# Performance work log

Hardware: AMD Instinct MI355X
Metric: run time of the kernel (lower is better)

## Reference

```python
import jax, jax.numpy as jnp
import numpy as np

EMBED = 1024
HEADS = 16
HEAD_DIM = EMBED // HEADS


def setup_inputs() -> dict:
    key = jax.random.key(0)
    k1, k2, k3, k4, k5 = jax.random.split(key, 5)
    B, S = 4, 2048
    scale = 1.0 / np.sqrt(EMBED)
    return {
        "query_features": jax.random.normal(k1, (B, S, EMBED), dtype=jnp.float32),
        "W_qkv": jax.random.normal(k2, (EMBED, 3 * EMBED), dtype=jnp.float32) * scale,
        "b_qkv": jnp.zeros((3 * EMBED,), dtype=jnp.float32),
        "W_out": jax.random.normal(k3, (EMBED, EMBED), dtype=jnp.float32) * scale,
        "b_out": jnp.zeros((EMBED,), dtype=jnp.float32),
    }


def reference(query_features, W_qkv, b_qkv, W_out, b_out):
    B, S, E = query_features.shape
    qkv = jnp.einsum("bse,ef->bsf", query_features, W_qkv) + b_qkv  # [B,S,3E]
    q, k, v = jnp.split(qkv, 3, axis=-1)
    # split heads: [B,H,S,D]
    def heads(x):
        return x.reshape(B, S, HEADS, HEAD_DIM).transpose(0, 2, 1, 3)
    q, k, v = heads(q), heads(k), heads(v)
    scale = 1.0 / np.sqrt(HEAD_DIM)
    scores = jnp.einsum("bhqd,bhkd->bhqk", q, k) * scale
    attn = jax.nn.softmax(scores, axis=-1)
    out = jnp.einsum("bhqk,bhkd->bhqd", attn, v)  # [B,H,S,D]
    out = out.transpose(0, 2, 1, 3).reshape(B, S, E)
    return jnp.einsum("bse,ef->bsf", out, W_out) + b_out
```

## Files before the change

### kernel.cpp

```cpp
#include <hip/hip_runtime.h>
#include <hip/hip_bf16.h>
#include <stdint.h>
#include <stddef.h>

using short8  = __attribute__((ext_vector_type(8))) short;
using short4v = __attribute__((ext_vector_type(4))) short;
using int4v   = __attribute__((ext_vector_type(4))) int;
using f32x4   = __attribute__((ext_vector_type(4))) float;
typedef __hip_bfloat16 bf16_t;

__device__ __forceinline__ void glds16(const void* g, const void* l) {
  __builtin_amdgcn_global_load_lds(
      (const __attribute__((address_space(1))) void*)g,
      (__attribute__((address_space(3))) void*)l, 16, 0, 0);
}
__device__ __forceinline__ short bfbits(float x) {
  bf16_t h = __float2bfloat16(x);
  return __builtin_bit_cast(short, h);
}
__device__ __forceinline__ int pk2(float lo, float hi) {
  return __builtin_amdgcn_perm(__builtin_bit_cast(unsigned, hi),
                               __builtin_bit_cast(unsigned, lo), 0x07060302u);
}

__global__ __launch_bounds__(256)
void preprocess(const void* __restrict__ Wqkv, bf16_t* __restrict__ WqkvT,
                const void* __restrict__ Wout, bf16_t* __restrict__ WoutT,
                const void* __restrict__ Xv, bf16_t* __restrict__ Xb,
                int* __restrict__ flag) {
  __shared__ int sbad;
  __shared__ float tile[32][33];
  const int tid = threadIdx.x;
  const int bid = blockIdx.x;
  if (tid == 0) sbad = 0;
  __syncthreads();
  {
    int bad = 0;
    const unsigned short* wp = (const unsigned short*)Wqkv;
#pragma unroll
    for (int j = 0; j < 4; ++j) {
      float f = __uint_as_float((unsigned)wp[tid + j * 256] << 16);
      if (!(fabsf(f) <= 1e10f)) bad = 1;
    }
    if (bad) sbad = 1;
  }
  __syncthreads();
  const int isf = sbad;
  if (bid == 0 && tid == 0) *flag = isf;

  if (bid < 4096) {
    int bx = bid & 127;
    const int by = bid >> 7;
    const int tx = tid & 31, ty = tid >> 5;
    const void* Wv;
    bf16_t* Wt;
    int C;
    if (bx < 96) {
      Wv = Wqkv; Wt = WqkvT; C = 3072;
    } else {
      bx -= 96; Wv = Wout; Wt = WoutT; C = 1024;
    }
    const int n0 = bx * 32, k0 = by * 32;
#pragma unroll
    for (int j = 0; j < 4; ++j) {
      const int k = k0 + ty + j * 8;
      tile[ty + j * 8][tx] =
          isf ? ((const float*)Wv)[(size_t)k * C + n0 + tx]
              : __bfloat162float(((const bf16_t*)Wv)[(size_t)k * C + n0 + tx]);
    }
    __syncthreads();
#pragma unroll
    for (int j = 0; j < 4; ++j) {
      const int n = n0 + ty + j * 8;
      Wt[(size_t)n * 1024 + k0 + tx] = __float2bfloat16(tile[tx][ty + j * 8]);
    }
  } else {
    const int i = ((bid - 4096) * 256 + tid) * 4;
    if (isf) {
      const float4 v = *(const float4*)((const float*)Xv + i);
      Xb[i + 0] = __float2bfloat16(v.x);
      Xb[i + 1] = __float2bfloat16(v.y);
      Xb[i + 2] = __float2bfloat16(v.z);
      Xb[i + 3] = __float2bfloat16(v.w);
    } else {
      *(uint2*)(Xb + i) = *(const uint2*)((const bf16_t*)Xv + i);
    }
  }
}

template <int MODE>
__global__ __launch_bounds__(256)
void gemm_k(const bf16_t* __restrict__ A, const bf16_t* __restrict__ Bt,
            const void* __restrict__ biasv, void* __restrict__ Cv,
            bf16_t* __restrict__ Qo, bf16_t* __restrict__ Ko,
            bf16_t* __restrict__ Vo, int M, int N, int K,
            const int* __restrict__ flag) {
  constexpr float CSC = 0.18033688011112042f;
  __shared__ __align__(16) bf16_t lA[2][128 * 64];
  __shared__ __align__(16) bf16_t lB[2][128 * 64];

  const int isf32 = *flag;
  const int tid  = threadIdx.x;
  const int w    = tid >> 6;
  const int lane = tid & 63;
  const int lrow = lane & 15;
  const int quad = lane >> 4;
  const int m0 = blockIdx.x * 128;
  const int n0 = blockIdx.y * 128;
  const int wm = (w >> 1) * 64;
  const int wn = (w & 1) * 64;

  f32x4 acc[4][4];
  for (int i = 0; i < 4; ++i)
    for (int j = 0; j < 4; ++j)
      for (int r = 0; r < 4; ++r) acc[i][j][r] = 0.f;

  const char* Ab = (const char*)A;
  const char* Bb = (const char*)Bt;
  unsigned aoff[4], boff[4];
  int ldst[4];
#pragma unroll
  for (int i = 0; i < 4; ++i) {
    const int cbase = i * 256 + w * 64;
    const int c = cbase + lane;
    const int row = c >> 3;
    const int q = (c & 7) ^ (row & 7);
    aoff[i] = (unsigned)((m0 + row) * K + q * 8) * 2u;
    boff[i] = (unsigned)((n0 + row) * K + q * 8) * 2u;
    ldst[i] = cbase * 16;
  }

  auto stage = [&](int buf, int kt) {
    const unsigned kb = (unsigned)kt * 2u;
#pragma unroll
    for (int i = 0; i < 4; ++i) {
      glds16(Ab + aoff[i] + kb, (const char*)lA[buf] + ldst[i]);
      glds16(Bb + boff[i] + kb, (const char*)lB[buf] + ldst[i]);
    }
  };

  stage(0, 0);
  __syncthreads();

  int buf = 0;
  for (int kt = 0; kt < K; kt += 64) {
    if (kt + 64 < K) stage(buf ^ 1, kt + 64);
    const char* la = (const char*)lA[buf];
    const char* lb = (const char*)lB[buf];
#pragma unroll
    for (int ks = 0; ks < 2; ++ks) {
      short8 af[4], bfr[4];
#pragma unroll
      for (int mi = 0; mi < 4; ++mi) {
        const int row = wm + mi * 16 + lrow;
        const int slot = (ks * 4 + quad) ^ (row & 7);
        af[mi] = *(const short8*)(la + row * 128 + slot * 16);
      }
#pragma unroll
      for (int ni = 0; ni < 4; ++ni) {
        const int row = wn + ni * 16 + lrow;
        const int slot = (ks * 4 + quad) ^ (row & 7);
        bfr[ni] = *(const short8*)(lb + row * 128 + slot * 16);
      }
#pragma unroll
      for (int mi = 0; mi < 4; ++mi)
#pragma unroll
        for (int ni = 0; ni < 4; ++ni)
          acc[mi][ni] = __builtin_amdgcn_mfma_f32_16x16x32_bf16(
              af[mi], bfr[ni], acc[mi][ni], 0, 0, 0);
    }
    __syncthreads();
    buf ^= 1;
  }

  if (MODE == 1) {
    const int sec = n0 >> 10;
    const int b = m0 >> 11;
    const int s0 = (m0 & 2047) + wm + quad * 4;
#pragma unroll
    for (int mi = 0; mi < 4; ++mi) {
#pragma unroll
      for (int ni = 0; ni < 4; ++ni) {
        const int col = n0 + wn + ni * 16 + lrow;
        const float bv = isf32 ? ((const float*)biasv)[col]
                               : __bfloat162float(((const bf16_t*)biasv)[col]);
        const int h = (col >> 6) & 15, d = col & 63;
        const int s = s0 + mi * 16;
        if (sec == 2) {
          short4v hv4;
#pragma unroll
          for (int r = 0; r < 4; ++r) hv4[r] = bfbits(acc[mi][ni][r] + bv);
          *(short4v*)(Vo + ((((size_t)b * 16 + h) * 64) + d) * 2048 + s) = hv4;
        } else if (sec == 0) {
          bf16_t* dst = Qo + ((((size_t)b * 16 + h) * 2048) + s) * 64 + d;
#pragma unroll
          for (int r = 0; r < 4; ++r)
            dst[(size_t)r * 64] = __float2bfloat16((acc[mi][ni][r] + bv) * CSC);
        } else {
          bf16_t* dst = Ko + ((((size_t)b * 16 + h) * 2048) + s) * 64 + d;
#pragma unroll
          for (int r = 0; r < 4; ++r)
            dst[(size_t)r * 64] = __float2bfloat16(acc[mi][ni][r] + bv);
        }
      }
    }
  } else {
#pragma unroll
    for (int mi = 0; mi < 4; ++mi) {
#pragma unroll
      for (int ni = 0; ni < 4; ++ni) {
        const int col = n0 + wn + ni * 16 + lrow;
        const float bv = isf32 ? ((const float*)biasv)[col]
                               : __bfloat162float(((const bf16_t*)biasv)[col]);
#pragma unroll
        for (int r = 0; r < 4; ++r) {
          const int row = m0 + wm + mi * 16 + quad * 4 + r;
          const float val = acc[mi][ni][r] + bv;
          if (isf32)
            ((float*)Cv)[(size_t)row * N + col] = val;
          else
            ((bf16_t*)Cv)[(size_t)row * N + col] = __float2bfloat16(val);
        }
      }
    }
  }
}

__global__ __launch_bounds__(256, 2)
void attn_fwd(const bf16_t* __restrict__ Q, const bf16_t* __restrict__ K,
              const bf16_t* __restrict__ Vt, bf16_t* __restrict__ AO) {
  __shared__ __align__(16) bf16_t lK[2][64 * 64];
  __shared__ __align__(16) bf16_t lV[2][64 * 64];

  const int tid  = threadIdx.x;
  const int w    = tid >> 6;
  const int lane = tid & 63;
  const int lrow = lane & 15;
  const int quad = lane >> 4;
  const int id = blockIdx.x;
  const int swz = (id & 7) * 64 + (id >> 3);
  const int bh  = swz >> 3;
  const int q0  = (swz & 7) * 256;

  const bf16_t* Qb = Q + (size_t)bh * 2048 * 64;
  const char* Kbc = (const char*)(K + (size_t)bh * 2048 * 64);
  const char* Vbc = (const char*)(Vt + (size_t)bh * 64 * 2048);

  const int rbase = (lrow >> 2) * 8 + (lrow & 3);
  const int fkl   = 2 * (lrow >> 2) + (lrow & 1);

  short8 aq[4][2];
#pragma unroll
  for (int qt = 0; qt < 4; ++qt)
#pragma unroll
    for (int ks = 0; ks < 2; ++ks)
      aq[qt][ks] = *(const short8*)(Qb +
          (size_t)(q0 + w * 64 + qt * 16 + lrow) * 64 + ks * 32 + quad * 8);

  short8 ones;
#pragma unroll
  for (int j = 0; j < 8; ++j) ones[j] = (short)0x3F80;

  const f32x4 zf = {0.f, 0.f, 0.f, 0.f};

  f32x4 ot[4][4];
  f32x4 lsacc[4];
#pragma unroll
  for (int dt = 0; dt < 4; ++dt)
#pragma unroll
    for (int qt = 0; qt < 4; ++qt)
#pragma unroll
      for (int r = 0; r < 4; ++r) ot[dt][qt][r] = 0.f;
#pragma unroll
  for (int qt = 0; qt < 4; ++qt)
#pragma unroll
    for (int r = 0; r < 4; ++r) lsacc[qt][r] = 0.f;

  unsigned kgo[2], vgo[2];
  int ldst[2];
#pragma unroll
  for (int i = 0; i < 2; ++i) {
    const int cbase = i * 256 + w * 64;
    const int c = cbase + lane;
    const int row = c >> 3, ch = c & 7;
    const int fk = 2 * ((row >> 3) & 3) + (row & 1);
    kgo[i] = (unsigned)(row * 128 + (ch ^ fk) * 16);
    vgo[i] = (unsigned)(row * 4096 + (ch ^ (row & 7)) * 16);
    ldst[i] = cbase * 16;
  }

  auto stage = [&](int buf, int cidx) {
    const unsigned kb = (unsigned)cidx * 8192u;
    const unsigned vb = (unsigned)cidx * 128u;
#pragma unroll
    for (int i = 0; i < 2; ++i) {
      glds16(Kbc + kgo[i] + kb, (const char*)lK[buf] + ldst[i]);
      glds16(Vbc + vgo[i] + vb, (const char*)lV[buf] + ldst[i]);
    }
  };

  auto compute = [&](const bf16_t* lKb, const bf16_t* lVb) {
#pragma unroll
    for (int g = 0; g < 2; ++g) {
      short8 ak0[2], ak1[2];
#pragma unroll
      for (int T = 0; T < 2; ++T) {
        const int row = g * 32 + T * 4 + rbase;
        ak0[T] = *(const short8*)((const char*)lKb + row * 128 +
                                  ((0 * 4 + quad) ^ fkl) * 16);
        ak1[T] = *(const short8*)((const char*)lKb + row * 128 +
                                  ((1 * 4 + quad) ^ fkl) * 16);
      }
      f32x4 sc[2][4];
      __builtin_amdgcn_s_setprio(1);
#pragma unroll
      for (int T = 0; T < 2; ++T)
#pragma unroll
        for (int qt = 0; qt < 4; ++qt)
          sc[T][qt] = __builtin_amdgcn_mfma_f32_16x16x32_bf16(
              ak0[T], aq[qt][0], zf, 0, 0, 0);
#pragma unroll
      for (int T = 0; T < 2; ++T)
#pragma unroll
        for (int qt = 0; qt < 4; ++qt)
          sc[T][qt] = __builtin_amdgcn_mfma_f32_16x16x32_bf16(
              ak1[T], aq[qt][1], sc[T][qt], 0, 0, 0);
      __builtin_amdgcn_s_setprio(0);

      short8 pb[4];
#pragma unroll
      for (int qt = 0; qt < 4; ++qt) {
        float p[8];
#pragma unroll
        for (int T = 0; T < 2; ++T)
#pragma unroll
          for (int r = 0; r < 4; ++r)
            p[T * 4 + r] = __builtin_amdgcn_exp2f(sc[T][qt][r]);
        int4v pi = {pk2(p[0], p[1]), pk2(p[2], p[3]), pk2(p[4], p[5]),
                    pk2(p[6], p[7])};
        pb[qt] = __builtin_bit_cast(short8, pi);
      }

      __builtin_amdgcn_s_setprio(1);
#pragma unroll
      for (int qt = 0; qt < 4; ++qt)
        lsacc[qt] = __builtin_amdgcn_mfma_f32_16x16x32_bf16(ones, pb[qt],
                                                            lsacc[qt], 0, 0, 0);
#pragma unroll
      for (int dt = 0; dt < 4; ++dt) {
        const int row = dt * 16 + lrow;
        const int slot = (g * 4 + quad) ^ (row & 7);
        const short8 vf =
            *(const short8*)((const char*)lVb + row * 128 + slot * 16);
#pragma unroll
        for (int qt = 0; qt < 4; ++qt)
          ot[dt][qt] = __builtin_amdgcn_mfma_f32_16x16x32_bf16(
              vf, pb[qt], ot[dt][qt], 0, 0, 0);
      }
      __builtin_amdgcn_s_setprio(0);
    }
  };

  stage(0, 0);
  __syncthreads();

  for (int c = 0; c < 32; ++c) {
    if (c + 1 < 32) stage((c + 1) & 1, c + 1);
    compute(lK[c & 1], lV[c & 1]);
    __syncthreads();
  }

  const int b = bh >> 4, h = bh & 15;
#pragma unroll
  for (int qt = 0; qt < 4; ++qt) {
    const float inv = 1.f / lsacc[qt][0];
    const int srow = q0 + w * 64 + qt * 16 + lrow;
#pragma unroll
    for (int dt = 0; dt < 4; ++dt) {
      uint2 pack;
      short* ps = (short*)&pack;
#pragma unroll
      for (int r = 0; r < 4; ++r) ps[r] = bfbits(ot[dt][qt][r] * inv);
      *(uint2*)(AO + ((size_t)b * 2048 + srow) * 1024 + h * 64 + dt * 16 +
                quad * 4) = pack;
    }
  }
}

extern "C" void kernel_launch(void* const* d_in, const int* in_sizes, int n_in,
                              void* d_out, int out_size, void* d_ws,
                              size_t ws_size, hipStream_t stream) {
  const void* X    = d_in[0];
  const void* Wqkv = d_in[1];
  const void* bqkv = d_in[2];
  const void* Wout = d_in[3];
  const void* bout = d_in[4];

  char* ws = (char*)d_ws;
  bf16_t* WqkvT = (bf16_t*)(ws);
  bf16_t* WoutT = (bf16_t*)(ws + 6291456);
  bf16_t* Qw    = (bf16_t*)(ws + 8388608);
  bf16_t* Kw    = (bf16_t*)(ws + 25165824);
  bf16_t* Vw    = (bf16_t*)(ws + 41943040);
  bf16_t* AOw   = (bf16_t*)(ws + 58720256);
  bf16_t* Xbf   = AOw;
  int*    flag  = (int*)(ws + 75497472);

  preprocess<<<12288, 256, 0, stream>>>(Wqkv, WqkvT, Wout, WoutT, X, Xbf, flag);

  gemm_k<1><<<dim3(64, 24), 256, 0, stream>>>(Xbf, WqkvT, bqkv, nullptr, Qw,
                                              Kw, Vw, 8192, 3072, 1024, flag);
  attn_fwd<<<512, 256, 0, stream>>>(Qw, Kw, Vw, AOw);
  gemm_k<0><<<dim3(64, 8), 256, 0, stream>>>(AOw, WoutT, bout, d_out, nullptr,
                                             nullptr, nullptr, 8192, 1024, 1024,
                                             flag);
}
```

Before: 255.8 us.

## Batch QK^T MFMAs across both groups and unroll the double-buffer loop

Inside compute, the QK^T MFMAs for both 32-key groups now run before any exp/PV work, keeping scores in a larger sc[2][2][4] array. This gives the scheduler more independent MFMAs to overlap with LDS reads and exp. The main loop is unrolled by two so buffer indices are compile-time constants. Stage addressing is recomputed per call instead of using precomputed offsets. The larger live score array raises register pressure, which may hurt the 2-blocks-per-SIMD occupancy target.

```diff
diff --git a/kernel.cpp b/kernel.cpp
--- a/kernel.cpp
+++ b/kernel.cpp
@@ -243,8 +243,8 @@
   const int q0  = (swz & 7) * 256;
 
   const bf16_t* Qb = Q + (size_t)bh * 2048 * 64;
-  const char* Kbc = (const char*)(K + (size_t)bh * 2048 * 64);
-  const char* Vbc = (const char*)(Vt + (size_t)bh * 64 * 2048);
+  const bf16_t* Kb = K + (size_t)bh * 2048 * 64;
+  const bf16_t* Vb = Vt + (size_t)bh * 64 * 2048;
 
   const int rbase = (lrow >> 2) * 8 + (lrow & 3);
   const int fkl   = 2 * (lrow >> 2) + (lrow & 1);
@@ -276,30 +276,22 @@
 #pragma unroll
     for (int r = 0; r < 4; ++r) lsacc[qt][r] = 0.f;
 
-  unsigned kgo[2], vgo[2];
-  int ldst[2];
-#pragma unroll
-  for (int i = 0; i < 2; ++i) {
-    const int cbase = i * 256 + w * 64;
-    const int c = cbase + lane;
-    const int row = c >> 3, ch = c & 7;
-    const int fk = 2 * ((row >> 3) & 3) + (row & 1);
-    kgo[i] = (unsigned)(row * 128 + (ch ^ fk) * 16);
-    vgo[i] = (unsigned)(row * 4096 + (ch ^ (row & 7)) * 16);
-    ldst[i] = cbase * 16;
-  }
-
-  auto stage = [&](int buf, int cidx) {
-    const unsigned kb = (unsigned)cidx * 8192u;
-    const unsigned vb = (unsigned)cidx * 128u;
+  auto stage = [&](int buf, int kt) {
 #pragma unroll
     for (int i = 0; i < 2; ++i) {
-      glds16(Kbc + kgo[i] + kb, (const char*)lK[buf] + ldst[i]);
-      glds16(Vbc + vgo[i] + vb, (const char*)lV[buf] + ldst[i]);
+      const int cbase = i * 256 + w * 64;
+      const int c = cbase + lane;
+      const int row = c >> 3, ch = c & 7;
+      const int fk = 2 * ((row >> 3) & 3) + (row & 1);
+      glds16(Kb + (size_t)(kt + row) * 64 + (ch ^ fk) * 8,
+             (const char*)lK[buf] + cbase * 16);
+      glds16(Vb + (size_t)row * 2048 + kt + (ch ^ (row & 7)) * 8,
+             (const char*)lV[buf] + cbase * 16);
     }
   };
 
   auto compute = [&](const bf16_t* lKb, const bf16_t* lVb) {
+    f32x4 sc[2][2][4];
 #pragma unroll
     for (int g = 0; g < 2; ++g) {
       short8 ak0[2], ak1[2];
@@ -311,22 +303,23 @@
         ak1[T] = *(const short8*)((const char*)lKb + row * 128 +
                                   ((1 * 4 + quad) ^ fkl) * 16);
       }
-      f32x4 sc[2][4];
       __builtin_amdgcn_s_setprio(1);
 #pragma unroll
       for (int T = 0; T < 2; ++T)
 #pragma unroll
         for (int qt = 0; qt < 4; ++qt)
-          sc[T][qt] = __builtin_amdgcn_mfma_f32_16x16x32_bf16(
+          sc[g][T][qt] = __builtin_amdgcn_mfma_f32_16x16x32_bf16(
               ak0[T], aq[qt][0], zf, 0, 0, 0);
 #pragma unroll
       for (int T = 0; T < 2; ++T)
 #pragma unroll
         for (int qt = 0; qt < 4; ++qt)
-          sc[T][qt] = __builtin_amdgcn_mfma_f32_16x16x32_bf16(
-              ak1[T], aq[qt][1], sc[T][qt], 0, 0, 0);
+          sc[g][T][qt] = __builtin_amdgcn_mfma_f32_16x16x32_bf16(
+              ak1[T], aq[qt][1], sc[g][T][qt], 0, 0, 0);
       __builtin_amdgcn_s_setprio(0);
-
+    }
+#pragma unroll
+    for (int g = 0; g < 2; ++g) {
       short8 pb[4];
 #pragma unroll
       for (int qt = 0; qt < 4; ++qt) {
@@ -335,7 +328,7 @@
         for (int T = 0; T < 2; ++T)
 #pragma unroll
           for (int r = 0; r < 4; ++r)
-            p[T * 4 + r] = __builtin_amdgcn_exp2f(sc[T][qt][r]);
+            p[T * 4 + r] = __builtin_amdgcn_exp2f(sc[g][T][qt][r]);
         int4v pi = {pk2(p[0], p[1]), pk2(p[2], p[3]), pk2(p[4], p[5]),
                     pk2(p[6], p[7])};
         pb[qt] = __builtin_bit_cast(short8, pi);
@@ -364,9 +357,12 @@
   stage(0, 0);
   __syncthreads();
 
-  for (int c = 0; c < 32; ++c) {
-    if (c + 1 < 32) stage((c + 1) & 1, c + 1);
-    compute(lK[c & 1], lV[c & 1]);
+  for (int kt = 0; kt < 2048; kt += 128) {
+    if (kt + 64 < 2048) stage(1, kt + 64);
+    compute(lK[0], lV[0]);
+    __syncthreads();
+    if (kt + 128 < 2048) stage(0, kt + 128);
+    compute(lK[1], lV[1]);
     __syncthreads();
   }
 
```

New measurement: 258.1 us. Within noise of the previous version (+0.9%).
